# Optimization experiments

Hardware: AMD Instinct MI355X
Metric: run time of the kernel (lower is better)

The kernel has to match this reference:

```python
import jax, jax.numpy as jnp
import numpy as np

B, P, N, C = 4, 12, 1024, 64  # batch, past window, nodes, channels (in==hidden==out)


def setup_inputs() -> dict:
    key = jax.random.key(0)
    k1, k2, k3, k4, k5, k6 = jax.random.split(key, 6)
    x = jax.random.normal(k1, (B, P, N, C), dtype=jnp.float32)
    # float adjacency mask in {0,1}; force self-loops so no softmax row is empty
    A = jax.random.randint(k2, (B, P, N, N), 0, 2).astype(jnp.float32)
    A = A.at[..., jnp.arange(N), jnp.arange(N)].set(1.0)
    # learned params (nn.Linear stores weight as [out, in]; y = x @ W.T)
    W_emb = jax.random.normal(k3, (C, C), dtype=jnp.float32) / jnp.sqrt(jnp.float32(C))
    a1 = jax.random.normal(k4, (C,), dtype=jnp.float32)
    a2 = jax.random.normal(k5, (C,), dtype=jnp.float32)
    W_lin = jax.random.normal(k6, (C, C), dtype=jnp.float32) / jnp.sqrt(jnp.float32(C))
    return {"x": x, "A": A, "W_emb": W_emb, "a1": a1, "a2": a2, "W_lin": W_lin}


def reference(x, A, W_emb, a1, a2, W_lin):
    # x_emb = emb(x)  (bias-free linear)
    x_emb = jnp.einsum('bpnc,hc->bpnh', x, W_emb)            # [B,P,N,H]
    s1 = x_emb @ a1                                           # [B,P,N]
    s2 = x_emb @ a2                                           # [B,P,N]
    # additive GAT scores: a1_i + a2_j, broadcast instead of repeat
    z = jax.nn.leaky_relu(s1[..., :, None] + s2[..., None, :], 0.01)  # [B,P,N,N]
    z = jnp.where(A == 0.0, -jnp.inf, z)
    pi = jax.nn.softmax(z, axis=-1)                           # masked attention
    agg = jnp.einsum('bpij,bpjc->bpic', pi, x)                # weighted aggregation
    out = jax.nn.sigmoid(jnp.einsum('bpic,oc->bpio', agg, W_lin))
    return (out, A)
```

## Files before the change

kernel.cpp:

```cpp
#include <hip/hip_runtime.h>

typedef __attribute__((ext_vector_type(8))) __bf16 bf16x8;
typedef __attribute__((ext_vector_type(4))) float f32x4;

#define N_ 1024
#define C_ 64
#define BP_ 48

static __device__ __forceinline__ unsigned short f2bf(float f) {
    __bf16 b = (__bf16)f;
    return __builtin_bit_cast(unsigned short, b);
}
static __device__ __forceinline__ unsigned int pack2(float a, float b) {
    return (unsigned int)f2bf(a) | ((unsigned int)f2bf(b) << 16);
}

__global__ __launch_bounds__(256) void gat_pre(
    const float* __restrict__ x, const float* __restrict__ Wemb,
    const float* __restrict__ a1, const float* __restrict__ a2,
    float* __restrict__ s1g, float* __restrict__ s2g,
    unsigned short* __restrict__ xT, float* __restrict__ M2part)
{
    __shared__ float xs[64][65];
    __shared__ float vs[2][64];
    const int t = threadIdx.x, l = t & 63, w = t >> 6;
    const int j0 = blockIdx.x * 64;
    const int bp = blockIdx.y;

    if (w == 0) {
        float v1 = 0.f, v2 = 0.f;
        #pragma unroll 8
        for (int h = 0; h < 64; ++h) {
            float we = Wemb[h * 64 + l];
            v1 = fmaf(a1[h], we, v1);
            v2 = fmaf(a2[h], we, v2);
        }
        vs[0][l] = v1; vs[1][l] = v2;
    }
    const float* xb = x + ((size_t)bp * N_ + j0) * C_;
    #pragma unroll
    for (int it = 0; it < 16; ++it)
        xs[it * 4 + w][l] = xb[(it * 4 + w) * C_ + l];
    __syncthreads();

    const int jr = t >> 2, c0 = (t & 3) * 16;
    float p1 = 0.f, p2 = 0.f;
    #pragma unroll
    for (int k = 0; k < 16; ++k) {
        float xv = xs[jr][c0 + k];
        p1 = fmaf(xv, vs[0][c0 + k], p1);
        p2 = fmaf(xv, vs[1][c0 + k], p2);
    }
    p1 += __shfl_xor(p1, 1); p1 += __shfl_xor(p1, 2);
    p2 += __shfl_xor(p2, 1); p2 += __shfl_xor(p2, 2);
    if ((l & 3) == 0) {
        s1g[bp * N_ + j0 + jr] = p1;
        s2g[bp * N_ + j0 + jr] = p2;
    }
    float m = p2;
    m = fmaxf(m, __shfl_xor(m, 4));
    m = fmaxf(m, __shfl_xor(m, 8));
    m = fmaxf(m, __shfl_xor(m, 16));
    m = fmaxf(m, __shfl_xor(m, 32));
    if (l == 0) M2part[bp * 64 + blockIdx.x * 4 + w] = m;

    const int c = t >> 2, part = t & 3;
    unsigned int ow[8];
    #pragma unroll
    for (int k = 0; k < 16; k += 2) {
        unsigned int lo = f2bf(xs[part * 16 + k][c]);
        unsigned int hi = f2bf(xs[part * 16 + k + 1][c]);
        ow[k >> 1] = lo | (hi << 16);
    }
    uint4* dst = (uint4*)(xT + (size_t)bp * C_ * N_ + (size_t)c * N_ + j0 + part * 16);
    dst[0] = make_uint4(ow[0], ow[1], ow[2], ow[3]);
    dst[1] = make_uint4(ow[4], ow[5], ow[6], ow[7]);
}

__global__ __launch_bounds__(256, 3) void gat_fused(
    const float* __restrict__ Ag, float* __restrict__ outA,
    const unsigned short* __restrict__ xT,
    const float* __restrict__ s1g, const float* __restrict__ s2g,
    const float* __restrict__ M2part,
    const float* __restrict__ Wlin, float* __restrict__ out)
{
    __shared__ unsigned short Plds[4][16][72];
    __shared__ float s2lds[1024];
    __shared__ float lsLDS[4][16];

    const int t = threadIdx.x, l = t & 63, w = t >> 6;
    const int i15 = l & 15, q = l >> 4;
    const int lm = l & 15, g16 = l >> 4;
    const int bp = blockIdx.y;
    const int ibase = blockIdx.x * 64 + w * 16;

    *(f32x4*)&s2lds[4 * t] = *(const f32x4*)&s2g[bp * N_ + 4 * t];

    float m2v = M2part[bp * 64 + l];
    #pragma unroll
    for (int off = 32; off >= 1; off >>= 1)
        m2v = fmaxf(m2v, __shfl_xor(m2v, off));
    const float M2 = m2v;
    const float s1_l = s1g[bp * N_ + ibase + i15];

    float s1r[4], mvr[4];
    #pragma unroll
    for (int sr = 0; sr < 4; ++sr) {
        s1r[sr] = __shfl(s1_l, 4 * sr + g16);
        float zr = s1r[sr] + M2;
        mvr[sr] = fmaxf(zr, 0.01f * zr);
    }

    __syncthreads();

    const float* Arow = Ag + ((size_t)bp * N_ + ibase + g16) * N_ + 4 * lm;
    float* oArow = outA + ((size_t)bp * N_ + ibase + g16) * N_ + 4 * lm;
    const unsigned short* xTrow = xT + (size_t)bp * C_ * N_ + (size_t)i15 * N_ + q * 8;

    f32x4 acc[4] = {};
    float ls4[4] = {0.f, 0.f, 0.f, 0.f};

    f32x4 Aa[4], Ab[4];
    bf16x8 Xa[8], Xb[8];

#define LOADX(X, kk) do {                                                     \
    _Pragma("unroll")                                                         \
    for (int nt = 0; nt < 4; ++nt)                                            \
        _Pragma("unroll")                                                     \
        for (int s = 0; s < 2; ++s)                                           \
            X[s * 4 + nt] = *(const bf16x8*)&xTrow[(size_t)nt * 16 * N_ +     \
                                                   (kk) * 64 + s * 32];       \
    } while (0)

#define LOADA(Ax, kk) do {                                                    \
    const float* _p = Arow + (kk) * 64;                                       \
    _Pragma("unroll")                                                         \
    for (int r = 0; r < 4; ++r)                                               \
        Ax[r] = __builtin_nontemporal_load((const f32x4*)(_p + r * 4 * N_));  \
    } while (0)

#define DOSR(Av, sr, jrel) do {                                               \
    __builtin_nontemporal_store(Av, (f32x4*)(oArow + (sr) * 4 * N_ + (jrel)));\
    float e0, e1, e2, e3;                                                     \
    { float zz = s1r[sr] + s2v[0]; zz = fmaxf(zz, 0.01f * zz);                \
      e0 = (Av[0] != 0.f) ? __expf(zz - mvr[sr]) : 0.f; }                     \
    { float zz = s1r[sr] + s2v[1]; zz = fmaxf(zz, 0.01f * zz);                \
      e1 = (Av[1] != 0.f) ? __expf(zz - mvr[sr]) : 0.f; }                     \
    { float zz = s1r[sr] + s2v[2]; zz = fmaxf(zz, 0.01f * zz);                \
      e2 = (Av[2] != 0.f) ? __expf(zz - mvr[sr]) : 0.f; }                     \
    { float zz = s1r[sr] + s2v[3]; zz = fmaxf(zz, 0.01f * zz);                \
      e3 = (Av[3] != 0.f) ? __expf(zz - mvr[sr]) : 0.f; }                     \
    ls4[sr] += (e0 + e1) + (e2 + e3);                                         \
    *(uint2*)&Plds[w][4 * (sr) + g16][4 * lm] =                               \
        make_uint2(pack2(e0, e1), pack2(e2, e3)); } while (0)

#define CONSUME(X, Ac, kk) do {                                               \
    const int jrel = (kk) * 64;                                               \
    const f32x4 s2v = *(const f32x4*)&s2lds[jrel + 4 * lm];                   \
    DOSR(Ac[0], 0, jrel); DOSR(Ac[1], 1, jrel);                               \
    DOSR(Ac[2], 2, jrel); DOSR(Ac[3], 3, jrel);                               \
    _Pragma("unroll")                                                         \
    for (int s = 0; s < 2; ++s) {                                             \
        bf16x8 af = *(const bf16x8*)&Plds[w][i15][s * 32 + q * 8];            \
        _Pragma("unroll")                                                     \
        for (int nt = 0; nt < 4; ++nt)                                        \
            acc[nt] = __builtin_amdgcn_mfma_f32_16x16x32_bf16(af, X[s * 4 + nt], \
                                                              acc[nt], 0, 0, 0); \
    } } while (0)

    LOADX(Xa, 0); LOADA(Aa, 0);
    #pragma unroll 1
    for (int k = 0; k < 16; k += 2) {
        LOADX(Xb, k + 1); LOADA(Ab, k + 1);
        CONSUME(Xa, Aa, k);
        if (k + 2 < 16) { LOADX(Xa, k + 2); LOADA(Aa, k + 2); }
        CONSUME(Xb, Ab, k + 1);
    }
#undef LOADX
#undef LOADA
#undef DOSR
#undef CONSUME

    #pragma unroll
    for (int sr = 0; sr < 4; ++sr) {
        ls4[sr] += __shfl_xor(ls4[sr], 1);
        ls4[sr] += __shfl_xor(ls4[sr], 2);
        ls4[sr] += __shfl_xor(ls4[sr], 4);
        ls4[sr] += __shfl_xor(ls4[sr], 8);
    }
    if (lm == 0) {
        #pragma unroll
        for (int sr = 0; sr < 4; ++sr)
            lsLDS[w][4 * sr + g16] = ls4[sr];
    }
    const f32x4 lsq = *(const f32x4*)&lsLDS[w][4 * q];

    unsigned short* aggl = &Plds[w][0][0];
    #pragma unroll
    for (int nt = 0; nt < 4; ++nt)
        #pragma unroll
        for (int r = 0; r < 4; ++r)
            aggl[(q * 4 + r) * 72 + nt * 16 + i15] = f2bf(acc[nt][r] / lsq[r]);

    f32x4 d2[4] = {};
    #pragma unroll
    for (int s = 0; s < 2; ++s) {
        bf16x8 af = *(const bf16x8*)&aggl[i15 * 72 + s * 32 + q * 8];
        #pragma unroll
        for (int nt = 0; nt < 4; ++nt) {
            const float* wp = Wlin + (size_t)(nt * 16 + i15) * C_ + s * 32 + q * 8;
            f32x4 w0 = *(const f32x4*)wp;
            f32x4 w1 = *(const f32x4*)(wp + 4);
            bf16x8 bfr;
            #pragma unroll
            for (int jj = 0; jj < 4; ++jj) { bfr[jj] = (__bf16)w0[jj]; bfr[4 + jj] = (__bf16)w1[jj]; }
            d2[nt] = __builtin_amdgcn_mfma_f32_16x16x32_bf16(af, bfr, d2[nt], 0, 0, 0);
        }
    }
    float* orow = out + ((size_t)bp * N_ + ibase) * C_;
    #pragma unroll
    for (int nt = 0; nt < 4; ++nt)
        #pragma unroll
        for (int r = 0; r < 4; ++r)
            orow[(size_t)(q * 4 + r) * C_ + nt * 16 + i15] =
                1.f / (1.f + __expf(-d2[nt][r]));
}

extern "C" void kernel_launch(void* const* d_in, const int* in_sizes, int n_in,
                              void* d_out, int out_size, void* d_ws, size_t ws_size,
                              hipStream_t stream) {
    const float* x    = (const float*)d_in[0];
    const float* Ag   = (const float*)d_in[1];
    const float* Wemb = (const float*)d_in[2];
    const float* a1   = (const float*)d_in[3];
    const float* a2   = (const float*)d_in[4];
    const float* Wlin = (const float*)d_in[5];
    float* out  = (float*)d_out;
    float* outA = out + (size_t)BP_ * N_ * C_;

    float* s1g = (float*)d_ws;
    float* s2g = s1g + BP_ * N_;
    float* M2part = s2g + BP_ * N_;
    unsigned short* xT = (unsigned short*)(M2part + BP_ * 64);

    gat_pre<<<dim3(16, BP_), dim3(256), 0, stream>>>(x, Wemb, a1, a2,
                                                     s1g, s2g, xT, M2part);
    gat_fused<<<dim3(16, BP_), dim3(256), 0, stream>>>(Ag, outA, xT, s1g, s2g,
                                                       M2part, Wlin, out);
}
```

Baseline: 387.9 us.

## Build MFMA A-operand in registers via permuted x layout, drop P LDS round-trip

Writes x in a permuted bf16 layout so that each lane's softmax-numerator values map directly onto the MFMA A-fragment. Each lane now reads its own row's adjacency entries, and the exp values are packed into registers instead of going through an LDS staging buffer and back. The masking select becomes a multiply by A, which relies on A being exactly 0 or 1. The X double buffer is dropped in favour of a single buffer loaded just before use, which cuts register use but exposes more load latency. The per-row sum reduction also becomes simpler.

```diff
diff --git a/kernel.cpp b/kernel.cpp
--- a/kernel.cpp
+++ b/kernel.cpp
@@ -19,7 +19,7 @@
     const float* __restrict__ x, const float* __restrict__ Wemb,
     const float* __restrict__ a1, const float* __restrict__ a2,
     float* __restrict__ s1g, float* __restrict__ s2g,
-    unsigned short* __restrict__ xT, float* __restrict__ M2part)
+    unsigned short* __restrict__ xP, float* __restrict__ M2part)
 {
     __shared__ float xs[64][65];
     __shared__ float vs[2][64];
@@ -65,32 +65,31 @@
     if (l == 0) M2part[bp * 64 + blockIdx.x * 4 + w] = m;
 
     const int c = t >> 2, part = t & 3;
-    unsigned int ow[8];
-    #pragma unroll
-    for (int k = 0; k < 16; k += 2) {
-        unsigned int lo = f2bf(xs[part * 16 + k][c]);
-        unsigned int hi = f2bf(xs[part * 16 + k + 1][c]);
-        ow[k >> 1] = lo | (hi << 16);
-    }
-    uint4* dst = (uint4*)(xT + (size_t)bp * C_ * N_ + (size_t)c * N_ + j0 + part * 16);
-    dst[0] = make_uint4(ow[0], ow[1], ow[2], ow[3]);
-    dst[1] = make_uint4(ow[4], ow[5], ow[6], ow[7]);
+    unsigned short* dstb = xP + (size_t)bp * C_ * N_ + (size_t)c * N_ + j0 +
+                           (part >> 1) * 32 + (part & 1) * 4;
+    #pragma unroll
+    for (int m_ = 0; m_ < 4; ++m_) {
+        unsigned int lo = pack2(xs[part * 16 + 4 * m_ + 0][c],
+                                xs[part * 16 + 4 * m_ + 1][c]);
+        unsigned int hi = pack2(xs[part * 16 + 4 * m_ + 2][c],
+                                xs[part * 16 + 4 * m_ + 3][c]);
+        *(uint2*)&dstb[m_ * 8] = make_uint2(lo, hi);
+    }
 }
 
 __global__ __launch_bounds__(256, 3) void gat_fused(
     const float* __restrict__ Ag, float* __restrict__ outA,
-    const unsigned short* __restrict__ xT,
+    const unsigned short* __restrict__ xP,
     const float* __restrict__ s1g, const float* __restrict__ s2g,
     const float* __restrict__ M2part,
     const float* __restrict__ Wlin, float* __restrict__ out)
 {
-    __shared__ unsigned short Plds[4][16][72];
+    __shared__ unsigned short aggLDS[4][16][72];
     __shared__ float s2lds[1024];
     __shared__ float lsLDS[4][16];
 
     const int t = threadIdx.x, l = t & 63, w = t >> 6;
     const int i15 = l & 15, q = l >> 4;
-    const int lm = l & 15, g16 = l >> 4;
     const int bp = blockIdx.y;
     const int ibase = blockIdx.x * 64 + w * 16;
 
@@ -102,100 +101,100 @@
         m2v = fmaxf(m2v, __shfl_xor(m2v, off));
     const float M2 = m2v;
     const float s1_l = s1g[bp * N_ + ibase + i15];
-
-    float s1r[4], mvr[4];
-    #pragma unroll
-    for (int sr = 0; sr < 4; ++sr) {
-        s1r[sr] = __shfl(s1_l, 4 * sr + g16);
-        float zr = s1r[sr] + M2;
-        mvr[sr] = fmaxf(zr, 0.01f * zr);
-    }
+    const float zr = s1_l + M2;
+    const float mv = fmaxf(zr, 0.01f * zr);
 
     __syncthreads();
 
-    const float* Arow = Ag + ((size_t)bp * N_ + ibase + g16) * N_ + 4 * lm;
-    float* oArow = outA + ((size_t)bp * N_ + ibase + g16) * N_ + 4 * lm;
-    const unsigned short* xTrow = xT + (size_t)bp * C_ * N_ + (size_t)i15 * N_ + q * 8;
+    const float* Arow = Ag + ((size_t)bp * N_ + ibase + i15) * N_ + q * 4;
+    float* oArow = outA + ((size_t)bp * N_ + ibase + i15) * N_ + q * 4;
+    const unsigned short* xProw = xP + (size_t)bp * C_ * N_ + (size_t)i15 * N_ + q * 8;
 
     f32x4 acc[4] = {};
-    float ls4[4] = {0.f, 0.f, 0.f, 0.f};
+    float ls = 0.f;
 
     f32x4 Aa[4], Ab[4];
-    bf16x8 Xa[8], Xb[8];
-
-#define LOADX(X, kk) do {                                                     \
+    bf16x8 X[8];
+
+#define LOADX(kk) do {                                                        \
     _Pragma("unroll")                                                         \
     for (int nt = 0; nt < 4; ++nt)                                            \
         _Pragma("unroll")                                                     \
         for (int s = 0; s < 2; ++s)                                           \
-            X[s * 4 + nt] = *(const bf16x8*)&xTrow[(size_t)nt * 16 * N_ +     \
+            X[s * 4 + nt] = *(const bf16x8*)&xProw[(size_t)nt * 16 * N_ +     \
                                                    (kk) * 64 + s * 32];       \
     } while (0)
 
 #define LOADA(Ax, kk) do {                                                    \
     const float* _p = Arow + (kk) * 64;                                       \
     _Pragma("unroll")                                                         \
-    for (int r = 0; r < 4; ++r)                                               \
-        Ax[r] = __builtin_nontemporal_load((const f32x4*)(_p + r * 4 * N_));  \
+    for (int g = 0; g < 4; ++g)                                               \
+        Ax[g] = __builtin_nontemporal_load((const f32x4*)(_p + g * 16));      \
     } while (0)
 
-#define DOSR(Av, sr, jrel) do {                                               \
-    __builtin_nontemporal_store(Av, (f32x4*)(oArow + (sr) * 4 * N_ + (jrel)));\
-    float e0, e1, e2, e3;                                                     \
-    { float zz = s1r[sr] + s2v[0]; zz = fmaxf(zz, 0.01f * zz);                \
-      e0 = (Av[0] != 0.f) ? __expf(zz - mvr[sr]) : 0.f; }                     \
-    { float zz = s1r[sr] + s2v[1]; zz = fmaxf(zz, 0.01f * zz);                \
-      e1 = (Av[1] != 0.f) ? __expf(zz - mvr[sr]) : 0.f; }                     \
-    { float zz = s1r[sr] + s2v[2]; zz = fmaxf(zz, 0.01f * zz);                \
-      e2 = (Av[2] != 0.f) ? __expf(zz - mvr[sr]) : 0.f; }                     \
-    { float zz = s1r[sr] + s2v[3]; zz = fmaxf(zz, 0.01f * zz);                \
-      e3 = (Av[3] != 0.f) ? __expf(zz - mvr[sr]) : 0.f; }                     \
-    ls4[sr] += (e0 + e1) + (e2 + e3);                                         \
-    *(uint2*)&Plds[w][4 * (sr) + g16][4 * lm] =                               \
-        make_uint2(pack2(e0, e1), pack2(e2, e3)); } while (0)
-
-#define CONSUME(X, Ac, kk) do {                                               \
+#define CONSUME(Ac, kk) do {                                                  \
     const int jrel = (kk) * 64;                                               \
-    const f32x4 s2v = *(const f32x4*)&s2lds[jrel + 4 * lm];                   \
-    DOSR(Ac[0], 0, jrel); DOSR(Ac[1], 1, jrel);                               \
-    DOSR(Ac[2], 2, jrel); DOSR(Ac[3], 3, jrel);                               \
-    _Pragma("unroll")                                                         \
-    for (int s = 0; s < 2; ++s) {                                             \
-        bf16x8 af = *(const bf16x8*)&Plds[w][i15][s * 32 + q * 8];            \
+                        \
+    f32x4 Ev[4];                                                              \
+    _Pragma("unroll")                                                         \
+    for (int g = 0; g < 4; ++g) {                                             \
+        const f32x4 s2v = *(const f32x4*)&s2lds[jrel + g * 16 + q * 4];       \
         _Pragma("unroll")                                                     \
-        for (int nt = 0; nt < 4; ++nt)                                        \
-            acc[nt] = __builtin_amdgcn_mfma_f32_16x16x32_bf16(af, X[s * 4 + nt], \
-                                                              acc[nt], 0, 0, 0); \
-    } } while (0)
-
-    LOADX(Xa, 0); LOADA(Aa, 0);
+        for (int r = 0; r < 4; ++r) {                                         \
+            float zz = s1_l + s2v[r];                                         \
+            zz = fmaxf(zz, 0.01f * zz);                                       \
+            Ev[g][r] = __expf(zz - mv);                                       \
+        }                                                                     \
+    }                                                                         \
+                \
+    _Pragma("unroll")                                                         \
+    for (int g = 0; g < 4; ++g)                                               \
+        __builtin_nontemporal_store(Ac[g], (f32x4*)(oArow + jrel + g * 16));  \
+    f32x4 P[4];                                                               \
+    _Pragma("unroll")                                                         \
+    for (int g = 0; g < 4; ++g) {                                             \
+        _Pragma("unroll")                                                     \
+        for (int r = 0; r < 4; ++r) {                                         \
+            P[g][r] = Ac[g][r] * Ev[g][r];                                    \
+            ls += P[g][r];                                                    \
+        }                                                                     \
+    }                                                                         \
+    uint4 u0 = make_uint4(pack2(P[0][0], P[0][1]), pack2(P[0][2], P[0][3]),   \
+                          pack2(P[1][0], P[1][1]), pack2(P[1][2], P[1][3]));  \
+    uint4 u1 = make_uint4(pack2(P[2][0], P[2][1]), pack2(P[2][2], P[2][3]),   \
+                          pack2(P[3][0], P[3][1]), pack2(P[3][2], P[3][3]));  \
+    bf16x8 af0 = __builtin_bit_cast(bf16x8, u0);                              \
+    bf16x8 af1 = __builtin_bit_cast(bf16x8, u1);                              \
+    _Pragma("unroll")                                                         \
+    for (int nt = 0; nt < 4; ++nt)                                            \
+        acc[nt] = __builtin_amdgcn_mfma_f32_16x16x32_bf16(af0, X[nt],         \
+                                                          acc[nt], 0, 0, 0);  \
+    _Pragma("unroll")                                                         \
+    for (int nt = 0; nt < 4; ++nt)                                            \
+        acc[nt] = __builtin_amdgcn_mfma_f32_16x16x32_bf16(af1, X[4 + nt],     \
+                                                          acc[nt], 0, 0, 0);  \
+    } while (0)
+
+    LOADA(Aa, 0);
     #pragma unroll 1
     for (int k = 0; k < 16; k += 2) {
-        LOADX(Xb, k + 1); LOADA(Ab, k + 1);
-        CONSUME(Xa, Aa, k);
-        if (k + 2 < 16) { LOADX(Xa, k + 2); LOADA(Aa, k + 2); }
-        CONSUME(Xb, Ab, k + 1);
+        LOADX(k);
+        LOADA(Ab, k + 1);
+        CONSUME(Aa, k);
+        LOADX(k + 1);
+        if (k + 2 < 16) LOADA(Aa, k + 2);
+        CONSUME(Ab, k + 1);
     }
 #undef LOADX
 #undef LOADA
-#undef DOSR
 #undef CONSUME
 
-    #pragma unroll
-    for (int sr = 0; sr < 4; ++sr) {
-        ls4[sr] += __shfl_xor(ls4[sr], 1);
-        ls4[sr] += __shfl_xor(ls4[sr], 2);
-        ls4[sr] += __shfl_xor(ls4[sr], 4);
-        ls4[sr] += __shfl_xor(ls4[sr], 8);
-    }
-    if (lm == 0) {
-        #pragma unroll
-        for (int sr = 0; sr < 4; ++sr)
-            lsLDS[w][4 * sr + g16] = ls4[sr];
-    }
+    ls += __shfl_xor(ls, 16);
+    ls += __shfl_xor(ls, 32);
+    if (q == 0) lsLDS[w][i15] = ls;
     const f32x4 lsq = *(const f32x4*)&lsLDS[w][4 * q];
 
-    unsigned short* aggl = &Plds[w][0][0];
+    unsigned short* aggl = &aggLDS[w][0][0];
     #pragma unroll
     for (int nt = 0; nt < 4; ++nt)
         #pragma unroll
@@ -241,10 +240,10 @@
     float* s1g = (float*)d_ws;
     float* s2g = s1g + BP_ * N_;
     float* M2part = s2g + BP_ * N_;
-    unsigned short* xT = (unsigned short*)(M2part + BP_ * 64);
+    unsigned short* xP = (unsigned short*)(M2part + BP_ * 64);
 
     gat_pre<<<dim3(16, BP_), dim3(256), 0, stream>>>(x, Wemb, a1, a2,
-                                                     s1g, s2g, xT, M2part);
-    gat_fused<<<dim3(16, BP_), dim3(256), 0, stream>>>(Ag, outA, xT, s1g, s2g,
+                                                     s1g, s2g, xP, M2part);
+    gat_fused<<<dim3(16, BP_), dim3(256), 0, stream>>>(Ag, outA, xP, s1g, s2g,
                                                        M2part, Wlin, out);
 }
```

After: 417.7 us. 1.08x slower.
